# Kernel tuning notes

Measured on AMD Instinct MI355X. Metric: run time of the kernel, lower is better.

Reference implementation:

```python
import jax, jax.numpy as jnp
import numpy as np

B, T, IN, H, OUT, SIM = 256, 128, 128, 1024, 256, 4
EPS_BN = 1e-5
EPS_COS = 1e-8
NEG_SLOPE = 0.2


def setup_inputs() -> dict:
    key = jax.random.key(0)
    ks = jax.random.split(key, 12)
    rn = lambda k, s: jax.random.normal(k, s, dtype=jnp.float32) * 0.05
    return {
        "x": jax.random.normal(ks[0], (B, T, IN), dtype=jnp.float32),
        "W_emb": rn(ks[1], (H, IN)),
        "b_emb": jnp.zeros((H,), jnp.float32),
        "gamma": jnp.ones((H,), jnp.float32),
        "beta": jnp.zeros((H,), jnp.float32),
        "memory": jax.random.normal(ks[2], (1, T, H), dtype=jnp.float32),
        "w_ih_x": rn(ks[3], (3 * OUT, H)),
        "w_hh_x": rn(ks[4], (3 * OUT, OUT)),
        "b_ih_x": jnp.zeros((3 * OUT,), jnp.float32),
        "b_hh_x": jnp.zeros((3 * OUT,), jnp.float32),
        "w_ih_m": rn(ks[5], (3 * OUT, H)),
        "w_hh_m": rn(ks[6], (3 * OUT, OUT)),
        "b_ih_m": jnp.zeros((3 * OUT,), jnp.float32),
        "b_hh_m": jnp.zeros((3 * OUT,), jnp.float32),
        "W_sx": rn(ks[7], (SIM, OUT)),
        "b_sx": jnp.zeros((SIM,), jnp.float32),
        "W_sm": rn(ks[8], (SIM, OUT)),
        "b_sm": jnp.zeros((SIM,), jnp.float32),
    }


def _gru(x, h, w_ih, w_hh, b_ih, b_hh):
    # PyTorch GRUCell math
    gi = x @ w_ih.T + b_ih
    gh = h @ w_hh.T + b_hh
    i_r, i_z, i_n = jnp.split(gi, 3, axis=-1)
    h_r, h_z, h_n = jnp.split(gh, 3, axis=-1)
    r = jax.nn.sigmoid(i_r + h_r)
    z = jax.nn.sigmoid(i_z + h_z)
    n = jnp.tanh(i_n + r * h_n)
    return (1.0 - z) * n + z * h


def _forward(x, W_emb, b_emb, gamma, beta, memory,
             w_ih_x, w_hh_x, b_ih_x, b_hh_x,
             w_ih_m, w_hh_m, b_ih_m, b_hh_m,
             W_sx, b_sx, W_sm, b_sm):
    # embed + LeakyReLU(0.2)
    e = x @ W_emb.T + b_emb                                  # (B,T,H)
    e = jnp.where(e >= 0, e, NEG_SLOPE * e)
    # BatchNorm1d, training mode: per-channel stats over (B,T), biased var
    mean = jnp.mean(e, axis=(0, 1))
    var = jnp.mean((e - mean) ** 2, axis=(0, 1))
    e = (e - mean) * jax.lax.rsqrt(var + EPS_BN) * gamma + beta

    mem = memory[0]                                          # (T,H) shared across batch
    b = x.shape[0]

    def step(carry, inps):
        hx, hm = carry
        xt, mt = inps                                        # (B,H), (H,)
        mtb = jnp.broadcast_to(mt, (b, mt.shape[-1]))
        hx = _gru(xt, hx, w_ih_x, w_hh_x, b_ih_x, b_hh_x)    # (B,OUT)
        hm = _gru(mtb, hm, w_ih_m, w_hh_m, b_ih_m, b_hh_m)   # (B,OUT)
        # cosine-similarity addressing between sim_size projections
        qx = hx @ W_sx.T + b_sx                              # (B,SIM)
        qm = hm @ W_sm.T + b_sm
        num = jnp.sum(qx * qm, axis=-1)
        den = (jnp.maximum(jnp.linalg.norm(qx, axis=-1), EPS_COS)
               * jnp.maximum(jnp.linalg.norm(qm, axis=-1), EPS_COS))
        g = jax.nn.sigmoid(num / den)[:, None]               # gate in (0,1)
        out = g * hx + (1.0 - g) * hm
        return (hx, hm), out

    h0 = (jnp.zeros((b, OUT), e.dtype), jnp.zeros((b, OUT), e.dtype))
    (_, _), outs = jax.lax.scan(step, h0, (e.transpose(1, 0, 2), mem))
    return outs[-1].reshape(-1, OUT)                         # out of last timestep


def reference(x, W_emb, b_emb, gamma, beta, memory,
              w_ih_x, w_hh_x, b_ih_x, b_hh_x,
              w_ih_m, w_hh_m, b_ih_m, b_hh_m,
              W_sx, b_sx, W_sm, b_sm):
    return _forward(x, W_emb, b_emb, gamma, beta, memory,
                    w_ih_x, w_hh_x, b_ih_x, b_hh_x,
                    w_ih_m, w_hh_m, b_ih_m, b_hh_m,
                    W_sx, b_sx, W_sm, b_sm)
```

## Files before the change

### kernel.cpp

```cpp
#include <hip/hip_runtime.h>
#include <stdint.h>


typedef float  f32x4 __attribute__((ext_vector_type(4)));
typedef __bf16 bf16x8 __attribute__((ext_vector_type(8)));

#define B_   256
#define T_   128
#define IN_  128
#define H_   1024
#define OUT_ 256
#define M_   32768

static constexpr size_t OFF_XB    = 0;
static constexpr size_t OFF_WEMB  = 8388608;
static constexpr size_t OFF_WHX   = 8650752;
static constexpr size_t OFF_WHM   = 9043968;
static constexpr size_t OFF_SUM   = 9437184;
static constexpr size_t OFF_SSQ   = 9441280;
static constexpr size_t OFF_SCALE = 9445376;
static constexpr size_t OFF_CC    = 9449472;
static constexpr size_t OFF_BIASX = 9453568;
static constexpr size_t OFF_GIM   = 9457664;
static constexpr size_t OFF_EACT  = 9654272;
static constexpr size_t OFF_GI    = 76763136;
static constexpr size_t OFF_HXF   = 127094784;
static constexpr size_t OFF_HMF   = 127356928;
static constexpr size_t OFF_WPX   = 127373312;

__device__ __forceinline__ float sigmoidf_(float x) {
    return __builtin_amdgcn_rcpf(1.0f + __expf(-x));
}
__device__ __forceinline__ float tanhf_(float x) {
    return 1.0f - 2.0f * __builtin_amdgcn_rcpf(1.0f + __expf(2.0f * x));
}
__device__ __forceinline__ void gload_lds16(const void* g, void* l) {
    __builtin_amdgcn_global_load_lds(
        (const __attribute__((address_space(1))) unsigned int*)g,
        (__attribute__((address_space(3))) unsigned int*)l, 16, 0, 0);
}

__global__ void prep(const float* __restrict__ x, const float* __restrict__ wemb,
                     const float* __restrict__ whx, const float* __restrict__ whm,
                     __bf16* __restrict__ xb, __bf16* __restrict__ wembb,
                     __bf16* __restrict__ whxb, __bf16* __restrict__ whmb,
                     float* __restrict__ stats )
{
    long i = (long)blockIdx.x * 256 + threadIdx.x;
    if (i < 2048) stats[i] = 0.0f;
    if (i < 4194304)      xb[i] = (__bf16)x[i];
    else if (i < 4325376) wembb[i - 4194304] = (__bf16)wemb[i - 4194304];
    else if (i < 4521984) whxb[i - 4325376]  = (__bf16)whx[i - 4325376];
    else if (i < 4718592) whmb[i - 4521984]  = (__bf16)whm[i - 4521984];
}

template<int MODE>
__launch_bounds__(256)
__global__ void gemm_nt(const __bf16* __restrict__ A, const __bf16* __restrict__ Bm,
                        const float* __restrict__ bias, __bf16* __restrict__ C,
                        float* __restrict__ sums, float* __restrict__ ssqs,
                        int K, int N)
{
    __shared__ __bf16 As[128 * 40];
    __shared__ __bf16 Bs[128 * 40];
    const int tid  = threadIdx.x;
    const int lane = tid & 63;
    const int wv   = tid >> 6;
    const int wm   = wv >> 1, wn = wv & 1;
    const int l15  = lane & 15, quad = lane >> 4;
    const long m0 = (long)blockIdx.x * 128;
    const long n0 = (long)blockIdx.y * 128;
    const int srow  = tid >> 1;
    const int shalf = tid & 1;
    const __bf16* ag = A  + (m0 + srow) * K + shalf * 16;
    const __bf16* bg = Bm + (n0 + srow) * K + shalf * 16;

    const f32x4 fz = {0.f, 0.f, 0.f, 0.f};
    f32x4 acc[4][4];
#pragma unroll
    for (int i = 0; i < 4; i++)
#pragma unroll
        for (int j = 0; j < 4; j++) acc[i][j] = fz;

    bf16x8 a0 = *(const bf16x8*)(ag);
    bf16x8 a1 = *(const bf16x8*)(ag + 8);
    bf16x8 b0 = *(const bf16x8*)(bg);
    bf16x8 b1 = *(const bf16x8*)(bg + 8);

    for (int k0 = 0; k0 < K; k0 += 32) {
        __syncthreads();
        *(bf16x8*)(&As[srow * 40 + shalf * 16    ]) = a0;
        *(bf16x8*)(&As[srow * 40 + shalf * 16 + 8]) = a1;
        *(bf16x8*)(&Bs[srow * 40 + shalf * 16    ]) = b0;
        *(bf16x8*)(&Bs[srow * 40 + shalf * 16 + 8]) = b1;
        __syncthreads();
        if (k0 + 32 < K) {
            a0 = *(const bf16x8*)(ag + k0 + 32);
            a1 = *(const bf16x8*)(ag + k0 + 40);
            b0 = *(const bf16x8*)(bg + k0 + 32);
            b1 = *(const bf16x8*)(bg + k0 + 40);
        }
        bf16x8 af[4], bfr[4];
#pragma unroll
        for (int mt = 0; mt < 4; mt++)
            af[mt] = *(const bf16x8*)(&As[(wm * 64 + mt * 16 + l15) * 40 + quad * 8]);
#pragma unroll
        for (int nt = 0; nt < 4; nt++)
            bfr[nt] = *(const bf16x8*)(&Bs[(wn * 64 + nt * 16 + l15) * 40 + quad * 8]);
#pragma unroll
        for (int mt = 0; mt < 4; mt++)
#pragma unroll
            for (int nt = 0; nt < 4; nt++)
                acc[mt][nt] = __builtin_amdgcn_mfma_f32_16x16x32_bf16(af[mt], bfr[nt], acc[mt][nt], 0, 0, 0);
    }

#pragma unroll
    for (int nt = 0; nt < 4; nt++) {
        const long ncol = n0 + wn * 64 + nt * 16 + l15;
        const float bi = bias[ncol];
        float s = 0.f, ss = 0.f;
#pragma unroll
        for (int mt = 0; mt < 4; mt++) {
#pragma unroll
            for (int r = 0; r < 4; r++) {
                float v = acc[mt][nt][r] + bi;
                if (MODE == 0) v = (v >= 0.f) ? v : 0.2f * v;
                __bf16 hv = (__bf16)v;
                C[(m0 + wm * 64 + mt * 16 + quad * 4 + r) * (long)N + ncol] = hv;
                if (MODE == 0) { float fv = (float)hv; s += fv; ss += fv * fv; }
            }
        }
        if (MODE == 0) {
            s += __shfl_xor(s, 16);  ss += __shfl_xor(ss, 16);
            s += __shfl_xor(s, 32);  ss += __shfl_xor(ss, 32);
            if (lane < 16) {
                atomicAdd(&sums[n0 + wn * 64 + nt * 16 + lane], s);
                atomicAdd(&ssqs[n0 + wn * 64 + nt * 16 + lane], ss);
            }
        }
    }
}

__global__ void finalize_stats(const float* __restrict__ sums, const float* __restrict__ ssqs,
                               const float* __restrict__ gamma, const float* __restrict__ beta,
                               float* __restrict__ scale, float* __restrict__ cc)
{
    int h = threadIdx.x;
    const float inv = 1.0f / 32768.0f;
    float mean = sums[h] * inv;
    float var  = ssqs[h] * inv - mean * mean;
    float s    = rsqrtf(var + 1e-5f) * gamma[h];
    scale[h] = s;
    cc[h]    = beta[h] - mean * s;
}

__global__ void build_wp(const float* __restrict__ w_ih_x, const float* __restrict__ b_ih_x,
                         const float* __restrict__ b_hh_x, const float* __restrict__ scale,
                         const float* __restrict__ cc, __bf16* __restrict__ wpx,
                         float* __restrict__ biasx)
{
    const int j = blockIdx.x;
    const int lane = threadIdx.x;
    float accv = 0.f;
#pragma unroll
    for (int i = 0; i < 16; i++) {
        int h = i * 64 + lane;
        float w = w_ih_x[(long)j * 1024 + h];
        wpx[(long)j * 1024 + h] = (__bf16)(w * scale[h]);
        accv += cc[h] * w;
    }
    for (int off = 32; off; off >>= 1) accv += __shfl_xor(accv, off);
    if (lane == 0) biasx[j] = accv + b_ih_x[j] + (j < 512 ? b_hh_x[j] : 0.0f);
}

__global__ void build_gim(const float* __restrict__ memory, const float* __restrict__ w_ih_m,
                          const float* __restrict__ b_ih_m, const float* __restrict__ b_hh_m,
                          __bf16* __restrict__ gim)
{
    const int j = blockIdx.x;
    const int lane = threadIdx.x;
    float w[16];
#pragma unroll
    for (int i = 0; i < 16; i++) w[i] = w_ih_m[(long)j * 1024 + i * 64 + lane];
    const float bb = b_ih_m[j] + (j < 512 ? b_hh_m[j] : 0.0f);
    for (int t = 0; t < 128; t++) {
        float s = 0.f;
#pragma unroll
        for (int i = 0; i < 16; i++) s += w[i] * memory[(long)t * 1024 + i * 64 + lane];
        for (int off = 32; off; off >>= 1) s += __shfl_xor(s, off);
        if (lane == 0) gim[t * 768 + j] = (__bf16)(s + bb);
    }
}

__launch_bounds__(512)
__global__ void recurrence(const __bf16* __restrict__ gi, const __bf16* __restrict__ gim,
                           const __bf16* __restrict__ whx, const __bf16* __restrict__ whm,
                           const float* __restrict__ bhhx, const float* __restrict__ bhhm,
                           float* __restrict__ hxfin, float* __restrict__ hmfin)
{
    __shared__ __bf16 hxl[2][16 * 264];
    __shared__ __bf16 gil[16 * 776];
    const int wg   = blockIdx.x;
    const int tid  = threadIdx.x;
    const int lane = tid & 63;
    const int v    = tid >> 6;
    const int l15  = lane & 15, quad = lane >> 4;
    const bool isX = (wg < 16);
    const __bf16* wh    = isX ? whx : whm;
    const float*  bhh   = isX ? bhhx : bhhm;
    const __bf16* gbase = isX ? gi : gim;

    bf16x8 W[6][8];
#pragma unroll
    for (int nt = 0; nt < 6; nt++) {
        const int g = nt >> 1, ct = nt & 1;
        const long j = g * 256 + (v * 2 + ct) * 16 + l15;
#pragma unroll
        for (int kt = 0; kt < 8; kt++)
            W[nt][kt] = *(const bf16x8*)(wh + j * 256 + kt * 32 + quad * 8);
    }
    float bhhn[2];
#pragma unroll
    for (int ct = 0; ct < 2; ct++) bhhn[ct] = bhh[512 + v * 32 + ct * 16 + l15];

    for (int i = tid; i < 16 * 264; i += 512) hxl[0][i] = (__bf16)0.f;

    float st[8];
#pragma unroll
    for (int i = 0; i < 8; i++) st[i] = 0.f;

    const int r0 = v * 2, r1 = r0 + 1;
    const long grow0 = isX ? (long)((wg * 16 + r0) * 128) * 768 : 0;
    const long grow1 = isX ? (long)((wg * 16 + r1) * 128) * 768 : 0;

    __syncthreads();

    int cur = 0;
    for (int t = 0; t < 128; t++) {
        {
            const __bf16* p0 = gbase + grow0 + (long)t * 768;
            const __bf16* p1 = gbase + grow1 + (long)t * 768;
            gload_lds16(p0 + (long)lane * 8, &gil[r0 * 776]);
            gload_lds16(p1 + (long)lane * 8, &gil[r1 * 776]);
            if (lane < 32) {
                gload_lds16(p0 + 512 + (long)lane * 8, &gil[r0 * 776 + 512]);
                gload_lds16(p1 + 512 + (long)lane * 8, &gil[r1 * 776 + 512]);
            }
        }
        const f32x4 fz = {0.f, 0.f, 0.f, 0.f};
        f32x4 acc[6];
#pragma unroll
        for (int nt = 0; nt < 6; nt++) acc[nt] = fz;
        const __bf16* hxc = &hxl[cur][0];
#pragma unroll
        for (int kt = 0; kt < 8; kt++) {
            bf16x8 a = *(const bf16x8*)(hxc + l15 * 264 + kt * 32 + quad * 8);
#pragma unroll
            for (int nt = 0; nt < 6; nt++)
                acc[nt] = __builtin_amdgcn_mfma_f32_16x16x32_bf16(a, W[nt][kt], acc[nt], 0, 0, 0);
        }
        __syncthreads();

        const int nxt = cur ^ 1;
        __bf16* hxn = &hxl[nxt][0];
#pragma unroll
        for (int ct = 0; ct < 2; ct++) {
            const int ob = v * 32 + ct * 16 + l15;
#pragma unroll
            for (int r = 0; r < 4; r++) {
                const int row = quad * 4 + r;
                const float gr = (float)gil[row * 776 + ob];
                const float gz = (float)gil[row * 776 + 256 + ob];
                const float gn = (float)gil[row * 776 + 512 + ob];
                const float rg = sigmoidf_(gr + acc[ct][r]);
                const float zg = sigmoidf_(gz + acc[2 + ct][r]);
                const float ng = tanhf_(gn + rg * (acc[4 + ct][r] + bhhn[ct]));
                float h = st[ct * 4 + r];
                h = (1.f - zg) * ng + zg * h;
                st[ct * 4 + r] = h;
                hxn[row * 264 + ob] = (__bf16)h;
            }
        }
        __syncthreads();
        cur = nxt;
    }

    float* finp = isX ? (hxfin + (long)wg * 16 * 256) : hmfin;
#pragma unroll
    for (int ct = 0; ct < 2; ct++) {
        const int ob = v * 32 + ct * 16 + l15;
#pragma unroll
        for (int r = 0; r < 4; r++)
            finp[(quad * 4 + r) * 256 + ob] = st[ct * 4 + r];
    }
}

__global__ void finalize(const float* __restrict__ hxfin, const float* __restrict__ hmfin,
                         const float* __restrict__ W_sx, const float* __restrict__ b_sx,
                         const float* __restrict__ W_sm, const float* __restrict__ b_sm,
                         float* __restrict__ out)
{
    const int b = blockIdx.x;
    const int lane = threadIdx.x;
    float qx[4], qm[4];
#pragma unroll
    for (int s = 0; s < 4; s++) {
        float px = 0.f, pm = 0.f;
#pragma unroll
        for (int i = 0; i < 4; i++) {
            int h = i * 64 + lane;
            px += W_sx[s * 256 + h] * hxfin[b * 256 + h];
            pm += W_sm[s * 256 + h] * hmfin[h];
        }
        for (int off = 32; off; off >>= 1) { px += __shfl_xor(px, off); pm += __shfl_xor(pm, off); }
        qx[s] = px + b_sx[s];
        qm[s] = pm + b_sm[s];
    }
    float num = 0.f, nx = 0.f, nm = 0.f;
#pragma unroll
    for (int s = 0; s < 4; s++) { num += qx[s] * qm[s]; nx += qx[s] * qx[s]; nm += qm[s] * qm[s]; }
    const float den = fmaxf(sqrtf(nx), 1e-8f) * fmaxf(sqrtf(nm), 1e-8f);
    const float g = 1.0f / (1.0f + __expf(-num / den));
#pragma unroll
    for (int i = 0; i < 4; i++) {
        int h = i * 64 + lane;
        out[b * 256 + h] = g * hxfin[b * 256 + h] + (1.0f - g) * hmfin[h];
    }
}

extern "C" void kernel_launch(void* const* d_in, const int* in_sizes, int n_in,
                              void* d_out, int out_size, void* d_ws, size_t ws_size,
                              hipStream_t stream)
{
    (void)in_sizes; (void)n_in; (void)out_size; (void)ws_size;
    const float* x      = (const float*)d_in[0];
    const float* W_emb  = (const float*)d_in[1];
    const float* b_emb  = (const float*)d_in[2];
    const float* gamma  = (const float*)d_in[3];
    const float* beta   = (const float*)d_in[4];
    const float* memory = (const float*)d_in[5];
    const float* w_ih_x = (const float*)d_in[6];
    const float* w_hh_x = (const float*)d_in[7];
    const float* b_ih_x = (const float*)d_in[8];
    const float* b_hh_x = (const float*)d_in[9];
    const float* w_ih_m = (const float*)d_in[10];
    const float* w_hh_m = (const float*)d_in[11];
    const float* b_ih_m = (const float*)d_in[12];
    const float* b_hh_m = (const float*)d_in[13];
    const float* W_sx   = (const float*)d_in[14];
    const float* b_sx   = (const float*)d_in[15];
    const float* W_sm   = (const float*)d_in[16];
    const float* b_sm   = (const float*)d_in[17];
    float* out = (float*)d_out;
    char* ws = (char*)d_ws;

    __bf16* xb    = (__bf16*)(ws + OFF_XB);
    __bf16* wembb = (__bf16*)(ws + OFF_WEMB);
    __bf16* whxb  = (__bf16*)(ws + OFF_WHX);
    __bf16* whmb  = (__bf16*)(ws + OFF_WHM);
    float*  sums  = (float*)(ws + OFF_SUM);
    float*  ssqs  = (float*)(ws + OFF_SSQ);
    float*  scale = (float*)(ws + OFF_SCALE);
    float*  cc    = (float*)(ws + OFF_CC);
    float*  biasx = (float*)(ws + OFF_BIASX);
    __bf16* gim   = (__bf16*)(ws + OFF_GIM);
    __bf16* eact  = (__bf16*)(ws + OFF_EACT);
    __bf16* gi    = (__bf16*)(ws + OFF_GI);
    float*  hxf   = (float*)(ws + OFF_HXF);
    float*  hmf   = (float*)(ws + OFF_HMF);
    __bf16* wpx   = (__bf16*)(ws + OFF_WPX);

    prep<<<18432, 256, 0, stream>>>(x, W_emb, w_hh_x, w_hh_m, xb, wembb, whxb, whmb, sums);
    gemm_nt<0><<<dim3(256, 8), 256, 0, stream>>>(xb, wembb, b_emb, eact, sums, ssqs, 128, 1024);
    finalize_stats<<<1, 1024, 0, stream>>>(sums, ssqs, gamma, beta, scale, cc);
    build_wp<<<768, 64, 0, stream>>>(w_ih_x, b_ih_x, b_hh_x, scale, cc, wpx, biasx);
    build_gim<<<768, 64, 0, stream>>>(memory, w_ih_m, b_ih_m, b_hh_m, gim);
    gemm_nt<1><<<dim3(256, 6), 256, 0, stream>>>(eact, wpx, biasx, gi, sums, ssqs, 1024, 768);
    recurrence<<<17, 512, 0, stream>>>(gi, gim, whxb, whmb, b_hh_x, b_hh_m, hxf, hmf);
    finalize<<<256, 64, 0, stream>>>(hxf, hmf, W_sx, b_sx, W_sm, b_sm, out);
}
```

Baseline: 611.6 us.

## Double-buffer GRU input gates and use direct global-to-LDS loads in GEMM

Result: faster. 541.9 us (-11.4%).

```diff
diff --git a/kernel.cpp b/kernel.cpp
--- a/kernel.cpp
+++ b/kernel.cpp
@@ -61,8 +61,8 @@
                         float* __restrict__ sums, float* __restrict__ ssqs,
                         int K, int N)
 {
-    __shared__ __bf16 As[128 * 40];
-    __shared__ __bf16 Bs[128 * 40];
+    __shared__ __bf16 As[128 * 32];
+    __shared__ __bf16 Bs[128 * 32];
     const int tid  = threadIdx.x;
     const int lane = tid & 63;
     const int wv   = tid >> 6;
@@ -70,10 +70,19 @@
     const int l15  = lane & 15, quad = lane >> 4;
     const long m0 = (long)blockIdx.x * 128;
     const long n0 = (long)blockIdx.y * 128;
-    const int srow  = tid >> 1;
-    const int shalf = tid & 1;
-    const __bf16* ag = A  + (m0 + srow) * K + shalf * 16;
-    const __bf16* bg = Bm + (n0 + srow) * K + shalf * 16;
+
+    const int srow = lane >> 2;
+    const int scol = (lane & 3) * 8;
+    const __bf16* ag[2]; const __bf16* bg[2];
+    __bf16* al[2]; __bf16* bl[2];
+#pragma unroll
+    for (int j = 0; j < 2; j++) {
+        const int s = wv * 2 + j;
+        ag[j] = A  + (m0 + s * 16 + srow) * K + scol;
+        bg[j] = Bm + (n0 + s * 16 + srow) * K + scol;
+        al[j] = &As[s * 512];
+        bl[j] = &Bs[s * 512];
+    }
 
     const f32x4 fz = {0.f, 0.f, 0.f, 0.f};
     f32x4 acc[4][4];
@@ -82,31 +91,20 @@
 #pragma unroll
         for (int j = 0; j < 4; j++) acc[i][j] = fz;
 
-    bf16x8 a0 = *(const bf16x8*)(ag);
-    bf16x8 a1 = *(const bf16x8*)(ag + 8);
-    bf16x8 b0 = *(const bf16x8*)(bg);
-    bf16x8 b1 = *(const bf16x8*)(bg + 8);
-
     for (int k0 = 0; k0 < K; k0 += 32) {
         __syncthreads();
-        *(bf16x8*)(&As[srow * 40 + shalf * 16    ]) = a0;
-        *(bf16x8*)(&As[srow * 40 + shalf * 16 + 8]) = a1;
-        *(bf16x8*)(&Bs[srow * 40 + shalf * 16    ]) = b0;
-        *(bf16x8*)(&Bs[srow * 40 + shalf * 16 + 8]) = b1;
+        gload_lds16(ag[0] + k0, al[0]);
+        gload_lds16(ag[1] + k0, al[1]);
+        gload_lds16(bg[0] + k0, bl[0]);
+        gload_lds16(bg[1] + k0, bl[1]);
         __syncthreads();
-        if (k0 + 32 < K) {
-            a0 = *(const bf16x8*)(ag + k0 + 32);
-            a1 = *(const bf16x8*)(ag + k0 + 40);
-            b0 = *(const bf16x8*)(bg + k0 + 32);
-            b1 = *(const bf16x8*)(bg + k0 + 40);
-        }
         bf16x8 af[4], bfr[4];
 #pragma unroll
         for (int mt = 0; mt < 4; mt++)
-            af[mt] = *(const bf16x8*)(&As[(wm * 64 + mt * 16 + l15) * 40 + quad * 8]);
+            af[mt] = *(const bf16x8*)(&As[(wm * 64 + mt * 16 + l15) * 32 + quad * 8]);
 #pragma unroll
         for (int nt = 0; nt < 4; nt++)
-            bfr[nt] = *(const bf16x8*)(&Bs[(wn * 64 + nt * 16 + l15) * 40 + quad * 8]);
+            bfr[nt] = *(const bf16x8*)(&Bs[(wn * 64 + nt * 16 + l15) * 32 + quad * 8]);
 #pragma unroll
         for (int mt = 0; mt < 4; mt++)
 #pragma unroll
@@ -199,7 +197,7 @@
                            float* __restrict__ hxfin, float* __restrict__ hmfin)
 {
     __shared__ __bf16 hxl[2][16 * 264];
-    __shared__ __bf16 gil[16 * 776];
+    __shared__ __bf16 gil[2][16 * 776];
     const int wg   = blockIdx.x;
     const int tid  = threadIdx.x;
     const int lane = tid & 63;
@@ -233,20 +231,32 @@
     const long grow0 = isX ? (long)((wg * 16 + r0) * 128) * 768 : 0;
     const long grow1 = isX ? (long)((wg * 16 + r1) * 128) * 768 : 0;
 
+    {
+        const __bf16* p0 = gbase + grow0;
+        const __bf16* p1 = gbase + grow1;
+        gload_lds16(p0 + (long)lane * 8, &gil[0][r0 * 776]);
+        gload_lds16(p1 + (long)lane * 8, &gil[0][r1 * 776]);
+        if (lane < 32) {
+            gload_lds16(p0 + 512 + (long)lane * 8, &gil[0][r0 * 776 + 512]);
+            gload_lds16(p1 + 512 + (long)lane * 8, &gil[0][r1 * 776 + 512]);
+        }
+    }
     __syncthreads();
 
     int cur = 0;
     for (int t = 0; t < 128; t++) {
-        {
-            const __bf16* p0 = gbase + grow0 + (long)t * 768;
-            const __bf16* p1 = gbase + grow1 + (long)t * 768;
-            gload_lds16(p0 + (long)lane * 8, &gil[r0 * 776]);
-            gload_lds16(p1 + (long)lane * 8, &gil[r1 * 776]);
+        if (t < 127) {
+            const __bf16* p0 = gbase + grow0 + (long)(t + 1) * 768;
+            const __bf16* p1 = gbase + grow1 + (long)(t + 1) * 768;
+            __bf16* dst = &gil[(t + 1) & 1][0];
+            gload_lds16(p0 + (long)lane * 8, dst + r0 * 776);
+            gload_lds16(p1 + (long)lane * 8, dst + r1 * 776);
             if (lane < 32) {
-                gload_lds16(p0 + 512 + (long)lane * 8, &gil[r0 * 776 + 512]);
-                gload_lds16(p1 + 512 + (long)lane * 8, &gil[r1 * 776 + 512]);
+                gload_lds16(p0 + 512 + (long)lane * 8, dst + r0 * 776 + 512);
+                gload_lds16(p1 + 512 + (long)lane * 8, dst + r1 * 776 + 512);
             }
         }
+
         const f32x4 fz = {0.f, 0.f, 0.f, 0.f};
         f32x4 acc[6];
 #pragma unroll
@@ -259,24 +269,24 @@
             for (int nt = 0; nt < 6; nt++)
                 acc[nt] = __builtin_amdgcn_mfma_f32_16x16x32_bf16(a, W[nt][kt], acc[nt], 0, 0, 0);
         }
-        __syncthreads();
 
         const int nxt = cur ^ 1;
         __bf16* hxn = &hxl[nxt][0];
+        const __bf16* gcur = &gil[t & 1][0];
 #pragma unroll
         for (int ct = 0; ct < 2; ct++) {
             const int ob = v * 32 + ct * 16 + l15;
 #pragma unroll
             for (int r = 0; r < 4; r++) {
                 const int row = quad * 4 + r;
-                const float gr = (float)gil[row * 776 + ob];
-                const float gz = (float)gil[row * 776 + 256 + ob];
-                const float gn = (float)gil[row * 776 + 512 + ob];
+                const float gr = (float)gcur[row * 776 + ob];
+                const float gz = (float)gcur[row * 776 + 256 + ob];
+                const float gn = (float)gcur[row * 776 + 512 + ob];
                 const float rg = sigmoidf_(gr + acc[ct][r]);
                 const float zg = sigmoidf_(gz + acc[2 + ct][r]);
                 const float ng = tanhf_(gn + rg * (acc[4 + ct][r] + bhhn[ct]));
                 float h = st[ct * 4 + r];
-                h = (1.f - zg) * ng + zg * h;
+                h = ng + zg * (h - ng);
                 st[ct * 4 + r] = h;
                 hxn[row * 264 + ob] = (__bf16)h;
             }
```
